# Kernel optimization log

Measured on AMD Instinct MI355X. Metric: run time of the kernel, lower is better.

Reference implementation:

```python
import jax, jax.numpy as jnp
import numpy as np
from jax.scipy.linalg import solve_triangular
from jax.scipy.special import logsumexp

N, T, M, K = 16384, 60, 8, 2


def setup_inputs() -> dict:
    key = jax.random.key(0)
    k1, k2, k3, k4 = jax.random.split(key, 4)
    mu = jax.random.normal(k1, (N, T, M, K), dtype=jnp.float32)
    # Build SPD covariance: sigma = A A^T + 0.5 I (module runs cholesky on it)
    A = 0.3 * jax.random.normal(k2, (N, T, M, K, K), dtype=jnp.float32)
    sigma = A @ jnp.swapaxes(A, -1, -2) + 0.5 * jnp.eye(K, dtype=jnp.float32)
    pi = jax.random.normal(k3, (N, M), dtype=jnp.float32)
    x = jax.random.normal(k4, (N, T, K), dtype=jnp.float32)
    mask = jnp.ones((N, T), dtype=jnp.float32)
    return {"mu": mu, "sigma": sigma, "pi": pi, "x": x, "mask": mask}


def reference(mu, sigma, pi, x, mask):
    k = mu.shape[-1]
    LOG_2PI = 1.8378770664093453
    # batched small-matrix Cholesky: (N,T,m,k,k)
    L = jnp.linalg.cholesky(sigma)
    diff = x[:, :, None, :] - mu                       # (N,T,m,k)
    # triangular solve L z = diff -> Mahalanobis term
    z = solve_triangular(L, diff[..., None], lower=True)[..., 0]
    maha = jnp.sum(z * z, axis=-1)                     # (N,T,m)
    log_det = jnp.sum(jnp.log(jnp.diagonal(L, axis1=-2, axis2=-1)), axis=-1)
    mvn_lp = -0.5 * (k * LOG_2PI + maha) - log_det     # (N,T,m)
    # Categorical(logits=pi) -> normalized log-probs, broadcast over T
    log_pi = jax.nn.log_softmax(pi, axis=-1)[:, None, :]  # (N,1,m)
    gmm_lp = logsumexp(log_pi + mvn_lp, axis=-1)       # (N,T)
    comp_loss = -gmm_lp
    # mask_reduce_losses: per-timestep mean over valid batch entries, then sum
    n_pred = jnp.sum(mask, axis=0)                     # (T,)
    t_losses = jnp.sum(comp_loss * mask, axis=0) / n_pred
    return jnp.sum(t_losses)
```

## Files before the change

### kernel.cpp

```cpp
#include <hip/hip_runtime.h>

#define T_DIM 60
#define LOSS_BLOCKS 3840
#define ITERS 8
#define PARTIALS_OFF 64

__global__ void init_kernel(float* __restrict__ ws_npred) {
    int i = threadIdx.x;
    if (i < T_DIM) ws_npred[i] = 0.0f;
}

__global__ void npred_kernel(const float* __restrict__ mask,
                             float* __restrict__ ws_npred, int NT) {
    __shared__ float bins[T_DIM];
    for (int j = threadIdx.x; j < T_DIM; j += blockDim.x) bins[j] = 0.0f;
    __syncthreads();
    int stride = gridDim.x * blockDim.x;
    for (int i = blockIdx.x * blockDim.x + threadIdx.x; i < NT; i += stride) {
        int t = i % T_DIM;
        atomicAdd(&bins[t], mask[i]);
    }
    __syncthreads();
    for (int j = threadIdx.x; j < T_DIM; j += blockDim.x)
        atomicAdd(&ws_npred[j], bins[j]);
}

__global__ __launch_bounds__(256)
void loss_kernel(const float* __restrict__ mu,
                 const float* __restrict__ sigma,
                 const float* __restrict__ pi,
                 const float* __restrict__ x,
                 const float* __restrict__ mask,
                 const float* __restrict__ ws_npred,
                 float* __restrict__ ws_partials, int NT) {
    const float LOG_2PI = 1.8378770664093453f;
    const int OCTS = NT / 8;
    int tid = threadIdx.x;
    int g = blockIdx.x * 256 + tid;
    int l = g & 7;
    int oct = g >> 3;
    float acc = 0.0f;

#pragma unroll
    for (int it = 0; it < ITERS; ++it) {
        int e = it * OCTS + oct;
        int n = e / T_DIM;
        int t = e - n * T_DIM;

        float4 sg = ((const float4*)sigma)[(size_t)e * 8 + l];
        float2 m2 = ((const float2*)mu)[(size_t)e * 8 + l];
        float2 xv = ((const float2*)x)[e];
        float p   = pi[(size_t)n * 8 + l];
        float mk  = mask[e];
        float npr = ws_npred[t];

        float a = sg.x, b = sg.y, c = sg.w;
        float d1 = xv.x - m2.x, d2 = xv.y - m2.y;
        float det = a * c - b * b;
        float maha = (c * d1 * d1 - 2.0f * b * d1 * d2 + a * d2 * d2) / det;
        float lp = p - LOG_2PI - 0.5f * (maha + __logf(det));

        float mx = lp;
        mx = fmaxf(mx, __shfl_xor(mx, 1));
        mx = fmaxf(mx, __shfl_xor(mx, 2));
        mx = fmaxf(mx, __shfl_xor(mx, 4));
        float s = __expf(lp - mx);
        s += __shfl_xor(s, 1);
        s += __shfl_xor(s, 2);
        s += __shfl_xor(s, 4);
        float lse_num = mx + __logf(s);

        float pmx = p;
        pmx = fmaxf(pmx, __shfl_xor(pmx, 1));
        pmx = fmaxf(pmx, __shfl_xor(pmx, 2));
        pmx = fmaxf(pmx, __shfl_xor(pmx, 4));
        float ps = __expf(p - pmx);
        ps += __shfl_xor(ps, 1);
        ps += __shfl_xor(ps, 2);
        ps += __shfl_xor(ps, 4);
        float lse_pi = pmx + __logf(ps);

        if (l == 0)
            acc += (lse_pi - lse_num) * mk / npr;
    }

#pragma unroll
    for (int off = 32; off > 0; off >>= 1)
        acc += __shfl_down(acc, off);
    __shared__ float wsum[4];
    int lane = tid & 63;
    int wid = tid >> 6;
    if (lane == 0) wsum[wid] = acc;
    __syncthreads();
    if (tid == 0)
        ws_partials[blockIdx.x] = wsum[0] + wsum[1] + wsum[2] + wsum[3];
}

__global__ void finalize_kernel(const float* __restrict__ ws_partials,
                                float* __restrict__ out, int nblocks) {
    float s = 0.0f;
    for (int i = threadIdx.x; i < nblocks; i += blockDim.x)
        s += ws_partials[i];
#pragma unroll
    for (int off = 32; off > 0; off >>= 1)
        s += __shfl_down(s, off);
    __shared__ float wsum[4];
    int lane = threadIdx.x & 63;
    int wid = threadIdx.x >> 6;
    if (lane == 0) wsum[wid] = s;
    __syncthreads();
    if (threadIdx.x == 0)
        out[0] = wsum[0] + wsum[1] + wsum[2] + wsum[3];
}

extern "C" void kernel_launch(void* const* d_in, const int* in_sizes, int n_in,
                              void* d_out, int out_size, void* d_ws, size_t ws_size,
                              hipStream_t stream) {
    const float* mu    = (const float*)d_in[0];
    const float* sigma = (const float*)d_in[1];
    const float* pi    = (const float*)d_in[2];
    const float* x     = (const float*)d_in[3];
    const float* mask  = (const float*)d_in[4];
    float* out = (float*)d_out;
    float* ws_npred    = (float*)d_ws;
    float* ws_partials = (float*)d_ws + PARTIALS_OFF;

    int NT = in_sizes[4];

    hipLaunchKernelGGL(init_kernel, dim3(1), dim3(64), 0, stream, ws_npred);
    hipLaunchKernelGGL(npred_kernel, dim3(240), dim3(256), 0, stream,
                       mask, ws_npred, NT);
    hipLaunchKernelGGL(loss_kernel, dim3(LOSS_BLOCKS), dim3(256), 0, stream,
                       mu, sigma, pi, x, mask, ws_npred, ws_partials, NT);
    hipLaunchKernelGGL(finalize_kernel, dim3(1), dim3(256), 0, stream,
                       ws_partials, out, LOSS_BLOCKS);
}
```

Before: 250.3 us.

## Stage sigma/mu/x/mask tiles into LDS via async global_load_lds per block

Each block now owns a contiguous chunk of 256 (n,t) elements and bulk-copies its sigma, mu, x and mask slices into shared memory with 16-byte global_load_lds DMA before computing. Before, each block strided across the whole array in eight iterations. The goal is fully contiguous, wide loads that bypass VGPRs and give better streaming bandwidth. In exchange it uses about 50KB of LDS per block, which limits occupancy, and it relies on NT being an exact multiple of 256 with hardcoded sizes.

```diff
diff --git a/kernel.cpp b/kernel.cpp
--- a/kernel.cpp
+++ b/kernel.cpp
@@ -1,8 +1,9 @@
 #include <hip/hip_runtime.h>
+#include <stdint.h>
 
 #define T_DIM 60
+#define EPB 256
 #define LOSS_BLOCKS 3840
-#define ITERS 8
 #define PARTIALS_OFF 64
 
 __global__ void init_kernel(float* __restrict__ ws_npred) {
@@ -25,6 +26,12 @@
         atomicAdd(&ws_npred[j], bins[j]);
 }
 
+__device__ __forceinline__ void async_copy16(const void* g, void* l) {
+    __builtin_amdgcn_global_load_lds(
+        (const __attribute__((address_space(1))) void*)g,
+        (__attribute__((address_space(3))) void*)l, 16, 0, 0);
+}
+
 __global__ __launch_bounds__(256)
 void loss_kernel(const float* __restrict__ mu,
                  const float* __restrict__ sigma,
@@ -32,27 +39,66 @@
                  const float* __restrict__ x,
                  const float* __restrict__ mask,
                  const float* __restrict__ ws_npred,
-                 float* __restrict__ ws_partials, int NT) {
+                 float* __restrict__ ws_partials) {
+    __shared__ float s_sigma[EPB * 32];
+    __shared__ float s_mu[EPB * 16];
+    __shared__ float s_x[EPB * 2];
+    __shared__ float s_mask[EPB];
+    __shared__ float s_npred[T_DIM];
+    __shared__ float wsum[4];
+
     const float LOG_2PI = 1.8378770664093453f;
-    const int OCTS = NT / 8;
     int tid = threadIdx.x;
-    int g = blockIdx.x * 256 + tid;
-    int l = g & 7;
-    int oct = g >> 3;
+    int w = tid >> 6;
+    int lane = tid & 63;
+    int E0 = blockIdx.x * EPB;
+
+    if (tid < T_DIM) s_npred[tid] = ws_npred[tid];
+
+    {
+        const char* g = (const char*)sigma + (size_t)E0 * 128;
+        char* l = (char*)s_sigma;
+#pragma unroll
+        for (int k = 0; k < 8; ++k) {
+            size_t off = (size_t)(k * 4 + w) * 1024;
+            async_copy16(g + off + (size_t)lane * 16, l + off);
+        }
+    }
+    {
+        const char* g = (const char*)mu + (size_t)E0 * 64;
+        char* l = (char*)s_mu;
+#pragma unroll
+        for (int k = 0; k < 4; ++k) {
+            size_t off = (size_t)(k * 4 + w) * 1024;
+            async_copy16(g + off + (size_t)lane * 16, l + off);
+        }
+    }
+    if (w < 2) {
+        size_t off = (size_t)w * 1024;
+        async_copy16((const char*)x + (size_t)E0 * 8 + off + (size_t)lane * 16,
+                     (char*)s_x + off);
+    } else if (w == 2) {
+        async_copy16((const char*)mask + (size_t)E0 * 4 + (size_t)lane * 16,
+                     (char*)s_mask);
+    }
+    __syncthreads();
+
+    int l = lane & 7;
+    int oct = lane >> 3;
     float acc = 0.0f;
-
 #pragma unroll
-    for (int it = 0; it < ITERS; ++it) {
-        int e = it * OCTS + oct;
+    for (int it = 0; it < 8; ++it) {
+        int e_loc = w * 64 + it * 8 + oct;
+        int e = E0 + e_loc;
         int n = e / T_DIM;
         int t = e - n * T_DIM;
 
-        float4 sg = ((const float4*)sigma)[(size_t)e * 8 + l];
-        float2 m2 = ((const float2*)mu)[(size_t)e * 8 + l];
-        float2 xv = ((const float2*)x)[e];
+        float4 sg = ((const float4*)s_sigma)[e_loc * 8 + l];
+        float2 m2 = ((const float2*)s_mu)[e_loc * 8 + l];
+        float2 xv = ((const float2*)s_x)[e_loc];
         float p   = pi[(size_t)n * 8 + l];
-        float mk  = mask[e];
-        float npr = ws_npred[t];
+        float mk  = s_mask[e_loc];
+        float npr = s_npred[t];
 
         float a = sg.x, b = sg.y, c = sg.w;
         float d1 = xv.x - m2.x, d2 = xv.y - m2.y;
@@ -87,10 +133,7 @@
 #pragma unroll
     for (int off = 32; off > 0; off >>= 1)
         acc += __shfl_down(acc, off);
-    __shared__ float wsum[4];
-    int lane = tid & 63;
-    int wid = tid >> 6;
-    if (lane == 0) wsum[wid] = acc;
+    if (lane == 0) wsum[w] = acc;
     __syncthreads();
     if (tid == 0)
         ws_partials[blockIdx.x] = wsum[0] + wsum[1] + wsum[2] + wsum[3];
@@ -131,7 +174,7 @@
     hipLaunchKernelGGL(npred_kernel, dim3(240), dim3(256), 0, stream,
                        mask, ws_npred, NT);
     hipLaunchKernelGGL(loss_kernel, dim3(LOSS_BLOCKS), dim3(256), 0, stream,
-                       mu, sigma, pi, x, mask, ws_npred, ws_partials, NT);
+                       mu, sigma, pi, x, mask, ws_npred, ws_partials);
     hipLaunchKernelGGL(finalize_kernel, dim3(1), dim3(256), 0, stream,
                        ws_partials, out, LOSS_BLOCKS);
 }
```

Result: slower. 258.1 us (+3.1%).

## Fuse mask count into loss kernel with per-timestep partials and nontemporal loads

Applied to the files above, without the earlier changes.

The separate init and npred passes over the mask are removed. The loss kernel now accumulates per-timestep loss and mask sums in shared memory and writes them per block, and a per-timestep reduction kernel divides by the count before a final sum. Input loads become nontemporal. This cuts two launches and a dependent mask pass, at the cost of shared-memory atomics within the loss kernel, a larger partials workspace, and a fallback path used when the workspace is too small.

```diff
diff --git a/kernel.cpp b/kernel.cpp
--- a/kernel.cpp
+++ b/kernel.cpp
@@ -1,9 +1,118 @@
 #include <hip/hip_runtime.h>
 
 #define T_DIM 60
-#define LOSS_BLOCKS 3840
-#define ITERS 8
-#define PARTIALS_OFF 64
+
+typedef float v4f __attribute__((ext_vector_type(4)));
+typedef float v2f __attribute__((ext_vector_type(2)));
+
+__device__ __forceinline__ float oct_elem_loss(
+        int e, int l,
+        const float* __restrict__ mu, const float* __restrict__ sigma,
+        const float* __restrict__ pi, const float* __restrict__ x,
+        const float* __restrict__ mask, int* t_out, float* mk_out) {
+    const float LOG_2PI = 1.8378770664093453f;
+    int n = e / T_DIM;
+    int t = e - n * T_DIM;
+    v4f sg = __builtin_nontemporal_load(((const v4f*)sigma) + (size_t)e * 8 + l);
+    v2f m2 = __builtin_nontemporal_load(((const v2f*)mu) + (size_t)e * 8 + l);
+    v2f xv = __builtin_nontemporal_load(((const v2f*)x) + e);
+    float p  = pi[(size_t)n * 8 + l];
+    float mk = __builtin_nontemporal_load(mask + e);
+
+    float a = sg.x, b = sg.y, c = sg.w;
+    float d1 = xv.x - m2.x, d2 = xv.y - m2.y;
+    float det = a * c - b * b;
+    float maha = (c * d1 * d1 - 2.0f * b * d1 * d2 + a * d2 * d2) / det;
+    float lp = p - LOG_2PI - 0.5f * (maha + __logf(det));
+
+    float mx = lp;
+    mx = fmaxf(mx, __shfl_xor(mx, 1));
+    mx = fmaxf(mx, __shfl_xor(mx, 2));
+    mx = fmaxf(mx, __shfl_xor(mx, 4));
+    float s = __expf(lp - mx);
+    s += __shfl_xor(s, 1); s += __shfl_xor(s, 2); s += __shfl_xor(s, 4);
+    float lse_num = mx + __logf(s);
+
+    float pmx = p;
+    pmx = fmaxf(pmx, __shfl_xor(pmx, 1));
+    pmx = fmaxf(pmx, __shfl_xor(pmx, 2));
+    pmx = fmaxf(pmx, __shfl_xor(pmx, 4));
+    float ps = __expf(p - pmx);
+    ps += __shfl_xor(ps, 1); ps += __shfl_xor(ps, 2); ps += __shfl_xor(ps, 4);
+    float lse_pi = pmx + __logf(ps);
+
+    *t_out = t; *mk_out = mk;
+    return (lse_pi - lse_num) * mk;
+}
+
+__global__ __launch_bounds__(256)
+void loss_fused_kernel(const float* __restrict__ mu,
+                       const float* __restrict__ sigma,
+                       const float* __restrict__ pi,
+                       const float* __restrict__ x,
+                       const float* __restrict__ mask,
+                       float* __restrict__ loss_p,
+                       float* __restrict__ mask_p,
+                       int NT, int nblocks) {
+    __shared__ float bl[T_DIM], bm[T_DIM];
+    int tid = threadIdx.x;
+    if (tid < T_DIM) { bl[tid] = 0.0f; bm[tid] = 0.0f; }
+    __syncthreads();
+
+    const int OCTS = NT / 8;
+    int g = blockIdx.x * 256 + tid;
+    int l = g & 7;
+    int oct = g >> 3;
+
+#pragma unroll
+    for (int it = 0; it < 8; ++it) {
+        int e = it * OCTS + oct;
+        int t; float mk;
+        float v = oct_elem_loss(e, l, mu, sigma, pi, x, mask, &t, &mk);
+        if (l == 0) {
+            atomicAdd(&bl[t], v);
+            atomicAdd(&bm[t], mk);
+        }
+    }
+    __syncthreads();
+    if (tid < T_DIM) {
+        loss_p[(size_t)tid * nblocks + blockIdx.x] = bl[tid];
+        mask_p[(size_t)tid * nblocks + blockIdx.x] = bm[tid];
+    }
+}
+
+__global__ void reduce_t_kernel(const float* __restrict__ loss_p,
+                                const float* __restrict__ mask_p,
+                                float* __restrict__ tvals, int nblocks) {
+    int t = blockIdx.x;
+    const float* lrow = loss_p + (size_t)t * nblocks;
+    const float* mrow = mask_p + (size_t)t * nblocks;
+    float sl = 0.0f, sm = 0.0f;
+    for (int i = threadIdx.x; i < nblocks; i += blockDim.x) {
+        sl += lrow[i]; sm += mrow[i];
+    }
+#pragma unroll
+    for (int off = 32; off > 0; off >>= 1) {
+        sl += __shfl_down(sl, off); sm += __shfl_down(sm, off);
+    }
+    __shared__ float wl[4], wm[4];
+    int lane = threadIdx.x & 63, w = threadIdx.x >> 6;
+    if (lane == 0) { wl[w] = sl; wm[w] = sm; }
+    __syncthreads();
+    if (threadIdx.x == 0)
+        tvals[t] = (wl[0] + wl[1] + wl[2] + wl[3]) /
+                   (wm[0] + wm[1] + wm[2] + wm[3]);
+}
+
+__global__ void final_sum_kernel(const float* __restrict__ tvals,
+                                 float* __restrict__ out) {
+    int tid = threadIdx.x;
+    float s = (tid < T_DIM) ? tvals[tid] : 0.0f;
+#pragma unroll
+    for (int off = 32; off > 0; off >>= 1)
+        s += __shfl_down(s, off);
+    if (tid == 0) out[0] = s;
+}
 
 __global__ void init_kernel(float* __restrict__ ws_npred) {
     int i = threadIdx.x;
@@ -16,88 +125,49 @@
     for (int j = threadIdx.x; j < T_DIM; j += blockDim.x) bins[j] = 0.0f;
     __syncthreads();
     int stride = gridDim.x * blockDim.x;
-    for (int i = blockIdx.x * blockDim.x + threadIdx.x; i < NT; i += stride) {
-        int t = i % T_DIM;
-        atomicAdd(&bins[t], mask[i]);
-    }
+    for (int i = blockIdx.x * blockDim.x + threadIdx.x; i < NT; i += stride)
+        atomicAdd(&bins[i % T_DIM], mask[i]);
     __syncthreads();
     for (int j = threadIdx.x; j < T_DIM; j += blockDim.x)
         atomicAdd(&ws_npred[j], bins[j]);
 }
 
 __global__ __launch_bounds__(256)
-void loss_kernel(const float* __restrict__ mu,
-                 const float* __restrict__ sigma,
-                 const float* __restrict__ pi,
-                 const float* __restrict__ x,
-                 const float* __restrict__ mask,
-                 const float* __restrict__ ws_npred,
-                 float* __restrict__ ws_partials, int NT) {
-    const float LOG_2PI = 1.8378770664093453f;
+void loss_fb_kernel(const float* __restrict__ mu,
+                    const float* __restrict__ sigma,
+                    const float* __restrict__ pi,
+                    const float* __restrict__ x,
+                    const float* __restrict__ mask,
+                    const float* __restrict__ ws_npred,
+                    float* __restrict__ ws_partials, int NT) {
+    __shared__ float s_npred[T_DIM];
+    int tid = threadIdx.x;
+    if (tid < T_DIM) s_npred[tid] = ws_npred[tid];
+    __syncthreads();
     const int OCTS = NT / 8;
-    int tid = threadIdx.x;
     int g = blockIdx.x * 256 + tid;
-    int l = g & 7;
-    int oct = g >> 3;
+    int l = g & 7, oct = g >> 3;
     float acc = 0.0f;
-
-#pragma unroll
-    for (int it = 0; it < ITERS; ++it) {
+#pragma unroll
+    for (int it = 0; it < 8; ++it) {
         int e = it * OCTS + oct;
-        int n = e / T_DIM;
-        int t = e - n * T_DIM;
-
-        float4 sg = ((const float4*)sigma)[(size_t)e * 8 + l];
-        float2 m2 = ((const float2*)mu)[(size_t)e * 8 + l];
-        float2 xv = ((const float2*)x)[e];
-        float p   = pi[(size_t)n * 8 + l];
-        float mk  = mask[e];
-        float npr = ws_npred[t];
-
-        float a = sg.x, b = sg.y, c = sg.w;
-        float d1 = xv.x - m2.x, d2 = xv.y - m2.y;
-        float det = a * c - b * b;
-        float maha = (c * d1 * d1 - 2.0f * b * d1 * d2 + a * d2 * d2) / det;
-        float lp = p - LOG_2PI - 0.5f * (maha + __logf(det));
-
-        float mx = lp;
-        mx = fmaxf(mx, __shfl_xor(mx, 1));
-        mx = fmaxf(mx, __shfl_xor(mx, 2));
-        mx = fmaxf(mx, __shfl_xor(mx, 4));
-        float s = __expf(lp - mx);
-        s += __shfl_xor(s, 1);
-        s += __shfl_xor(s, 2);
-        s += __shfl_xor(s, 4);
-        float lse_num = mx + __logf(s);
-
-        float pmx = p;
-        pmx = fmaxf(pmx, __shfl_xor(pmx, 1));
-        pmx = fmaxf(pmx, __shfl_xor(pmx, 2));
-        pmx = fmaxf(pmx, __shfl_xor(pmx, 4));
-        float ps = __expf(p - pmx);
-        ps += __shfl_xor(ps, 1);
-        ps += __shfl_xor(ps, 2);
-        ps += __shfl_xor(ps, 4);
-        float lse_pi = pmx + __logf(ps);
-
-        if (l == 0)
-            acc += (lse_pi - lse_num) * mk / npr;
-    }
-
+        int t; float mk;
+        float v = oct_elem_loss(e, l, mu, sigma, pi, x, mask, &t, &mk);
+        if (l == 0) acc += v / s_npred[t];
+    }
 #pragma unroll
     for (int off = 32; off > 0; off >>= 1)
         acc += __shfl_down(acc, off);
     __shared__ float wsum[4];
-    int lane = tid & 63;
-    int wid = tid >> 6;
-    if (lane == 0) wsum[wid] = acc;
+    int lane = tid & 63, w = tid >> 6;
+    if (lane == 0) wsum[w] = acc;
     __syncthreads();
     if (tid == 0)
         ws_partials[blockIdx.x] = wsum[0] + wsum[1] + wsum[2] + wsum[3];
 }
 
-__global__ void finalize_kernel(const float* __restrict__ ws_partials,
-                                float* __restrict__ out, int nblocks) {
+__global__ void finalize_fb_kernel(const float* __restrict__ ws_partials,
+                                   float* __restrict__ out, int nblocks) {
     float s = 0.0f;
     for (int i = threadIdx.x; i < nblocks; i += blockDim.x)
         s += ws_partials[i];
@@ -105,9 +175,8 @@
     for (int off = 32; off > 0; off >>= 1)
         s += __shfl_down(s, off);
     __shared__ float wsum[4];
-    int lane = threadIdx.x & 63;
-    int wid = threadIdx.x >> 6;
-    if (lane == 0) wsum[wid] = s;
+    int lane = threadIdx.x & 63, w = threadIdx.x >> 6;
+    if (lane == 0) wsum[w] = s;
     __syncthreads();
     if (threadIdx.x == 0)
         out[0] = wsum[0] + wsum[1] + wsum[2] + wsum[3];
@@ -122,16 +191,31 @@
     const float* x     = (const float*)d_in[3];
     const float* mask  = (const float*)d_in[4];
     float* out = (float*)d_out;
-    float* ws_npred    = (float*)d_ws;
-    float* ws_partials = (float*)d_ws + PARTIALS_OFF;
+    float* ws = (float*)d_ws;
 
     int NT = in_sizes[4];
-
-    hipLaunchKernelGGL(init_kernel, dim3(1), dim3(64), 0, stream, ws_npred);
-    hipLaunchKernelGGL(npred_kernel, dim3(240), dim3(256), 0, stream,
-                       mask, ws_npred, NT);
-    hipLaunchKernelGGL(loss_kernel, dim3(LOSS_BLOCKS), dim3(256), 0, stream,
-                       mu, sigma, pi, x, mask, ws_npred, ws_partials, NT);
-    hipLaunchKernelGGL(finalize_kernel, dim3(1), dim3(256), 0, stream,
-                       ws_partials, out, LOSS_BLOCKS);
-}
+    int nblocks = NT / 256;
+    size_t need = ((size_t)2 * T_DIM * nblocks + 64) * sizeof(float);
+
+    if (ws_size >= need) {
+        float* loss_p = ws;
+        float* mask_p = ws + (size_t)T_DIM * nblocks;
+        float* tvals  = ws + (size_t)2 * T_DIM * nblocks;
+        hipLaunchKernelGGL(loss_fused_kernel, dim3(nblocks), dim3(256), 0, stream,
+                           mu, sigma, pi, x, mask, loss_p, mask_p, NT, nblocks);
+        hipLaunchKernelGGL(reduce_t_kernel, dim3(T_DIM), dim3(256), 0, stream,
+                           loss_p, mask_p, tvals, nblocks);
+        hipLaunchKernelGGL(final_sum_kernel, dim3(1), dim3(64), 0, stream,
+                           tvals, out);
+    } else {
+        float* ws_npred    = ws;
+        float* ws_partials = ws + 64;
+        hipLaunchKernelGGL(init_kernel, dim3(1), dim3(64), 0, stream, ws_npred);
+        hipLaunchKernelGGL(npred_kernel, dim3(240), dim3(256), 0, stream,
+                           mask, ws_npred, NT);
+        hipLaunchKernelGGL(loss_fb_kernel, dim3(nblocks), dim3(256), 0, stream,
+                           mu, sigma, pi, x, mask, ws_npred, ws_partials, NT);
+        hipLaunchKernelGGL(finalize_fb_kernel, dim3(1), dim3(256), 0, stream,
+                           ws_partials, out, nblocks);
+    }
+}
```

New measurement: 232.6 us. 7.1% less time.

## Fuse mask count into loss kernel with per-timestep partials and contiguous block tiling

Applied to the files above, without the earlier changes.

Removes the separate init and npred kernels. The loss kernel now accumulates per-timestep loss and mask sums in shared memory, writes per-block partials laid out by timestep, and a two-stage reduction divides by the mask count afterwards. Each block now handles a contiguous run of 256 elements instead of strided octets. The block computes log-sum-exp over pi once per row, drops the max subtraction in the component logsumexp, and uses nontemporal loads. The price is shared-memory atomics, a larger workspace, and a risk of exp overflow or underflow since the logsumexp is no longer stabilised.

```diff
diff --git a/kernel.cpp b/kernel.cpp
--- a/kernel.cpp
+++ b/kernel.cpp
@@ -1,58 +1,55 @@
 #include <hip/hip_runtime.h>
 
 #define T_DIM 60
-#define LOSS_BLOCKS 3840
-#define ITERS 8
-#define PARTIALS_OFF 64
+#define NBLK 3840
 
-__global__ void init_kernel(float* __restrict__ ws_npred) {
-    int i = threadIdx.x;
-    if (i < T_DIM) ws_npred[i] = 0.0f;
-}
+typedef float v4f __attribute__((ext_vector_type(4)));
+typedef float v2f __attribute__((ext_vector_type(2)));
 
-__global__ void npred_kernel(const float* __restrict__ mask,
-                             float* __restrict__ ws_npred, int NT) {
-    __shared__ float bins[T_DIM];
-    for (int j = threadIdx.x; j < T_DIM; j += blockDim.x) bins[j] = 0.0f;
-    __syncthreads();
-    int stride = gridDim.x * blockDim.x;
-    for (int i = blockIdx.x * blockDim.x + threadIdx.x; i < NT; i += stride) {
-        int t = i % T_DIM;
-        atomicAdd(&bins[t], mask[i]);
+__global__ __launch_bounds__(256)
+void loss_fused_kernel(const float* __restrict__ mu,
+                       const float* __restrict__ sigma,
+                       const float* __restrict__ pi,
+                       const float* __restrict__ x,
+                       const float* __restrict__ mask,
+                       float* __restrict__ loss_p,
+                       float* __restrict__ mask_p) {
+    __shared__ float bl[T_DIM], bm[T_DIM];
+    __shared__ float s_lsepi[8];
+    const float LOG_2PI = 1.8378770664093453f;
+    int tid = threadIdx.x;
+    int E0 = blockIdx.x * 256;
+    int n_base = E0 / T_DIM;
+    int ncnt = (E0 + 255) / T_DIM - n_base + 1;
+
+    if (tid < T_DIM) { bl[tid] = 0.0f; bm[tid] = 0.0f; }
+    if (tid < ncnt) {
+        const float* pr = pi + (size_t)(n_base + tid) * 8;
+        float q0 = pr[0], q1 = pr[1], q2 = pr[2], q3 = pr[3];
+        float q4 = pr[4], q5 = pr[5], q6 = pr[6], q7 = pr[7];
+        float mx = fmaxf(fmaxf(fmaxf(q0, q1), fmaxf(q2, q3)),
+                         fmaxf(fmaxf(q4, q5), fmaxf(q6, q7)));
+        float s = __expf(q0 - mx) + __expf(q1 - mx) + __expf(q2 - mx) +
+                  __expf(q3 - mx) + __expf(q4 - mx) + __expf(q5 - mx) +
+                  __expf(q6 - mx) + __expf(q7 - mx);
+        s_lsepi[tid] = mx + __logf(s);
     }
     __syncthreads();
-    for (int j = threadIdx.x; j < T_DIM; j += blockDim.x)
-        atomicAdd(&ws_npred[j], bins[j]);
-}
 
-__global__ __launch_bounds__(256)
-void loss_kernel(const float* __restrict__ mu,
-                 const float* __restrict__ sigma,
-                 const float* __restrict__ pi,
-                 const float* __restrict__ x,
-                 const float* __restrict__ mask,
-                 const float* __restrict__ ws_npred,
-                 float* __restrict__ ws_partials, int NT) {
-    const float LOG_2PI = 1.8378770664093453f;
-    const int OCTS = NT / 8;
-    int tid = threadIdx.x;
-    int g = blockIdx.x * 256 + tid;
-    int l = g & 7;
-    int oct = g >> 3;
-    float acc = 0.0f;
+    int l = tid & 7;
+    int oct = tid >> 3;
+    int e = E0 + oct;
+    int n = e / T_DIM;
+    int t = e - n * T_DIM;
+    int nb = n - n_base;
 
 #pragma unroll
-    for (int it = 0; it < ITERS; ++it) {
-        int e = it * OCTS + oct;
-        int n = e / T_DIM;
-        int t = e - n * T_DIM;
-
-        float4 sg = ((const float4*)sigma)[(size_t)e * 8 + l];
-        float2 m2 = ((const float2*)mu)[(size_t)e * 8 + l];
-        float2 xv = ((const float2*)x)[e];
-        float p   = pi[(size_t)n * 8 + l];
-        float mk  = mask[e];
-        float npr = ws_npred[t];
+    for (int it = 0; it < 8; ++it) {
+        v4f sg = __builtin_nontemporal_load((const v4f*)sigma + (size_t)e * 8 + l);
+        v2f m2 = __builtin_nontemporal_load((const v2f*)mu + (size_t)e * 8 + l);
+        v2f xv = __builtin_nontemporal_load((const v2f*)x + e);
+        float mk = __builtin_nontemporal_load(mask + e);
+        float p  = pi[(size_t)n * 8 + l];
 
         float a = sg.x, b = sg.y, c = sg.w;
         float d1 = xv.x - m2.x, d2 = xv.y - m2.y;
@@ -60,57 +57,59 @@
         float maha = (c * d1 * d1 - 2.0f * b * d1 * d2 + a * d2 * d2) / det;
         float lp = p - LOG_2PI - 0.5f * (maha + __logf(det));
 
-        float mx = lp;
-        mx = fmaxf(mx, __shfl_xor(mx, 1));
-        mx = fmaxf(mx, __shfl_xor(mx, 2));
-        mx = fmaxf(mx, __shfl_xor(mx, 4));
-        float s = __expf(lp - mx);
+        float s = __expf(lp);
         s += __shfl_xor(s, 1);
         s += __shfl_xor(s, 2);
         s += __shfl_xor(s, 4);
-        float lse_num = mx + __logf(s);
 
-        float pmx = p;
-        pmx = fmaxf(pmx, __shfl_xor(pmx, 1));
-        pmx = fmaxf(pmx, __shfl_xor(pmx, 2));
-        pmx = fmaxf(pmx, __shfl_xor(pmx, 4));
-        float ps = __expf(p - pmx);
-        ps += __shfl_xor(ps, 1);
-        ps += __shfl_xor(ps, 2);
-        ps += __shfl_xor(ps, 4);
-        float lse_pi = pmx + __logf(ps);
+        if (l == 0) {
+            float v = (s_lsepi[nb] - __logf(s)) * mk;
+            atomicAdd(&bl[t], v);
+            atomicAdd(&bm[t], mk);
+        }
 
-        if (l == 0)
-            acc += (lse_pi - lse_num) * mk / npr;
+        e += 32;
+        t += 32;
+        if (t >= T_DIM) { t -= T_DIM; n += 1; nb += 1; }
     }
-
-#pragma unroll
-    for (int off = 32; off > 0; off >>= 1)
-        acc += __shfl_down(acc, off);
-    __shared__ float wsum[4];
-    int lane = tid & 63;
-    int wid = tid >> 6;
-    if (lane == 0) wsum[wid] = acc;
     __syncthreads();
-    if (tid == 0)
-        ws_partials[blockIdx.x] = wsum[0] + wsum[1] + wsum[2] + wsum[3];
+    if (tid < T_DIM) {
+        loss_p[(size_t)tid * NBLK + blockIdx.x] = bl[tid];
+        mask_p[(size_t)tid * NBLK + blockIdx.x] = bm[tid];
+    }
 }
 
-__global__ void finalize_kernel(const float* __restrict__ ws_partials,
-                                float* __restrict__ out, int nblocks) {
-    float s = 0.0f;
-    for (int i = threadIdx.x; i < nblocks; i += blockDim.x)
-        s += ws_partials[i];
+__global__ void reduce_t_kernel(const float* __restrict__ loss_p,
+                                const float* __restrict__ mask_p,
+                                float* __restrict__ tvals, int nblocks) {
+    int t = blockIdx.x;
+    const float* lrow = loss_p + (size_t)t * nblocks;
+    const float* mrow = mask_p + (size_t)t * nblocks;
+    float sl = 0.0f, sm = 0.0f;
+    for (int i = threadIdx.x; i < nblocks; i += blockDim.x) {
+        sl += lrow[i]; sm += mrow[i];
+    }
+#pragma unroll
+    for (int off = 32; off > 0; off >>= 1) {
+        sl += __shfl_down(sl, off); sm += __shfl_down(sm, off);
+    }
+    __shared__ float wl[4], wm[4];
+    int lane = threadIdx.x & 63, w = threadIdx.x >> 6;
+    if (lane == 0) { wl[w] = sl; wm[w] = sm; }
+    __syncthreads();
+    if (threadIdx.x == 0)
+        tvals[t] = (wl[0] + wl[1] + wl[2] + wl[3]) /
+                   (wm[0] + wm[1] + wm[2] + wm[3]);
+}
+
+__global__ void final_sum_kernel(const float* __restrict__ tvals,
+                                 float* __restrict__ out) {
+    int tid = threadIdx.x;
+    float s = (tid < T_DIM) ? tvals[tid] : 0.0f;
 #pragma unroll
     for (int off = 32; off > 0; off >>= 1)
         s += __shfl_down(s, off);
-    __shared__ float wsum[4];
-    int lane = threadIdx.x & 63;
-    int wid = threadIdx.x >> 6;
-    if (lane == 0) wsum[wid] = s;
-    __syncthreads();
-    if (threadIdx.x == 0)
-        out[0] = wsum[0] + wsum[1] + wsum[2] + wsum[3];
+    if (tid == 0) out[0] = s;
 }
 
 extern "C" void kernel_launch(void* const* d_in, const int* in_sizes, int n_in,
@@ -122,16 +121,15 @@
     const float* x     = (const float*)d_in[3];
     const float* mask  = (const float*)d_in[4];
     float* out = (float*)d_out;
-    float* ws_npred    = (float*)d_ws;
-    float* ws_partials = (float*)d_ws + PARTIALS_OFF;
+    float* ws = (float*)d_ws;
+    float* loss_p = ws;
+    float* mask_p = ws + (size_t)T_DIM * NBLK;
+    float* tvals  = ws + (size_t)2 * T_DIM * NBLK;
 
-    int NT = in_sizes[4];
-
-    hipLaunchKernelGGL(init_kernel, dim3(1), dim3(64), 0, stream, ws_npred);
-    hipLaunchKernelGGL(npred_kernel, dim3(240), dim3(256), 0, stream,
-                       mask, ws_npred, NT);
-    hipLaunchKernelGGL(loss_kernel, dim3(LOSS_BLOCKS), dim3(256), 0, stream,
-                       mu, sigma, pi, x, mask, ws_npred, ws_partials, NT);
-    hipLaunchKernelGGL(finalize_kernel, dim3(1), dim3(256), 0, stream,
-                       ws_partials, out, LOSS_BLOCKS);
+    hipLaunchKernelGGL(loss_fused_kernel, dim3(NBLK), dim3(256), 0, stream,
+                       mu, sigma, pi, x, mask, loss_p, mask_p);
+    hipLaunchKernelGGL(reduce_t_kernel, dim3(T_DIM), dim3(256), 0, stream,
+                       loss_p, mask_p, tvals, NBLK);
+    hipLaunchKernelGGL(final_sum_kernel, dim3(1), dim3(64), 0, stream,
+                       tvals, out);
 }
```

Measured after the change: 230.1 us. 1.09x faster.
